# Kernel tuning notes

Measured on AMD Instinct MI355X. Metric: run time of the kernel, lower is better.

## Reference

```python
import jax, jax.numpy as jnp
import numpy as np

H = 128   # hidden_size
B = 8
TQ = 512  # num queries
TK = 512  # num keys


def setup_inputs() -> dict:
    key = jax.random.key(0)
    ks = jax.random.split(key, 8)
    s = 1.0 / np.sqrt(H)  # torch Linear default init bound
    return {
        "queries": jax.random.normal(ks[0], (B, TQ, H), dtype=jnp.float32),
        "keys": jax.random.normal(ks[1], (B, TK, H), dtype=jnp.float32),
        "Wa_w": jax.random.uniform(ks[2], (H, H), jnp.float32, -s, s),
        "Wa_b": jax.random.uniform(ks[3], (H,), jnp.float32, -s, s),
        "Ua_w": jax.random.uniform(ks[4], (H, H), jnp.float32, -s, s),
        "Ua_b": jax.random.uniform(ks[5], (H,), jnp.float32, -s, s),
        "Va_w": jax.random.uniform(ks[6], (H,), jnp.float32, -s, s),
        "Va_b": jax.random.uniform(ks[7], (), jnp.float32, -s, s),
    }


def reference(queries, keys, Wa_w, Wa_b, Ua_w, Ua_b, Va_w, Va_b):
    # Linear projections (torch Linear: y = x @ W.T + b)
    q = queries @ Wa_w.T + Wa_b                  # (B, Tq, H)
    k = keys @ Ua_w.T + Ua_b                     # (B, Tk, H)
    # Additive (Bahdanau) scores with broadcast intermediate (B, Tq, Tk, H)
    e = jnp.tanh(q[:, :, None, :] + k[:, None, :, :])
    scores = jnp.einsum('bqkh,h->bqk', e, Va_w) + Va_b  # (B, Tq, Tk)
    weights = jax.nn.softmax(scores, axis=-1)            # softmax over keys
    contexts = jnp.einsum('bqk,bkh->bqh', weights, keys) # (B, Tq, H)
    return contexts, weights
```

## Files before the change

### kernel.cpp

```cpp
#include <hip/hip_runtime.h>
#include <hip/hip_bf16.h>
#include <stdint.h>

#define HD 128
#define NB 8
#define TQN 512
#define TKN 512
#define QT 8
#define KTILE 64
#define KSTR 132
#define QSTR 132
#define KBSTR 136
#define FQT 8

typedef __attribute__((ext_vector_type(8))) short short8;
typedef __attribute__((ext_vector_type(4))) float f32x4;
typedef __attribute__((ext_vector_type(2))) float f32x2;

#if __has_builtin(__builtin_elementwise_fma)
#define FMA2(a,b,c) __builtin_elementwise_fma((a),(b),(c))
#else
#define FMA2(a,b,c) ((a)*(b)+(c))
#endif

static __device__ __forceinline__ float lo16(uint32_t w){
  union { uint32_t i; float f; } v; v.i = w << 16; return v.f;
}
static __device__ __forceinline__ float hi16(uint32_t w){
  union { uint32_t i; float f; } v; v.i = w & 0xffff0000u; return v.f;
}
static __device__ __forceinline__ float bf2f(unsigned short u){
  union { uint32_t i; float f; } v; v.i = ((uint32_t)u) << 16; return v.f;
}
static __device__ __forceinline__ uint32_t f2bf(float f){
  union { float f; uint32_t i; } v; v.f = f;
  uint32_t u = v.i;
  u += 0x7fffu + ((u >> 16) & 1u);
  return u >> 16;
}
static __device__ __forceinline__ float tanh_acc(float x){
  float e = __builtin_amdgcn_exp2f(x * 2.8853900817779268f);
  return fmaf(-2.0f, __builtin_amdgcn_rcpf(e + 1.0f), 1.0f);
}
template<int CTRL>
static __device__ __forceinline__ float dpp_add(float x){
  union { float f; int i; } u; u.f = x;
  int y = __builtin_amdgcn_update_dpp(0, u.i, CTRL, 0xf, 0xf, true);
  union { int i; float f; } w; w.i = y;
  return x + w.f;
}
static __device__ __forceinline__ float ld1(const void* p, size_t idx, bool f32){
  return f32 ? ((const float*)p)[idx] : bf2f(((const unsigned short*)p)[idx]);
}
static __device__ __forceinline__ short8 ld8bf(const void* p, size_t idx, bool f32){
  short8 r;
  if (f32){
    const float* s = (const float*)p + idx;
    #pragma unroll
    for (int i = 0; i < 8; i++) r[i] = (short)f2bf(s[i]);
  } else {
    r = *(const short8*)((const unsigned short*)p + idx);
  }
  return r;
}

__global__ __launch_bounds__(256) void proj_kernel(
    const void* __restrict__ queries, const void* __restrict__ keys,
    const void* __restrict__ Wa_w,   const void* __restrict__ Wa_b,
    const void* __restrict__ Ua_w,   const void* __restrict__ Ua_b,
    float* __restrict__ tq_g, unsigned short* __restrict__ tk_gb)
{
  __shared__ unsigned int flg_s[8];
  const int tid = threadIdx.x;
  if (tid < 8) flg_s[tid] = 0;
  __syncthreads();
  {
    const void* ptrs[6] = {queries, keys, Wa_w, Wa_b, Ua_w, Ua_b};
    const int grp = tid >> 5;
    const int l   = tid & 31;
    if (grp < 6){
      const unsigned short* p = (const unsigned short*)ptrs[grp];
      unsigned short a = p[2*l], c = p[64 + 2*l];
      if (((a >> 7) & 0xFF) > 0x90 || ((c >> 7) & 0xFF) > 0x90)
        atomicOr(&flg_s[grp], 1u);
    }
  }
  __syncthreads();
  const int lane = tid & 63, wv = tid >> 6, ln = lane & 15, quad = lane >> 4;
  const int b7  = blockIdx.x & 7;
  const int idx = blockIdx.x >> 3;
  const int row0 = (idx < 32) ? (b7*TQN + idx*16)
                              : (NB*TQN + b7*TKN + (idx-32)*16);

  const void* x; const void* W; const void* bias; int r;
  bool fx, fw, fb;
  const bool isK = (row0 >= NB*TQN);
  if (!isK){
    x = queries; W = Wa_w; bias = Wa_b; r = row0;
    fx = flg_s[0] != 0; fw = flg_s[2] != 0; fb = flg_s[3] != 0;
  } else {
    x = keys; W = Ua_w; bias = Ua_b; r = row0 - NB*TQN;
    fx = flg_s[1] != 0; fw = flg_s[4] != 0; fb = flg_s[5] != 0;
  }

  short8 a[4];
  #pragma unroll
  for (int ks = 0; ks < 4; ks++)
    a[ks] = ld8bf(x, (size_t)(r + ln)*HD + ks*32 + quad*8, fx);

  #pragma unroll
  for (int nt = 0; nt < 2; nt++){
    const int h0 = (2*wv + nt)*16;
    f32x4 c = {0.f,0.f,0.f,0.f};
    #pragma unroll
    for (int ks = 0; ks < 4; ks++)
      c = __builtin_amdgcn_mfma_f32_16x16x32_bf16(
            a[ks], ld8bf(W, (size_t)(h0 + ln)*HD + ks*32 + quad*8, fw), c, 0,0,0);
    const float wb = ld1(bias, h0 + ln, fb);
    #pragma unroll
    for (int r4 = 0; r4 < 4; r4++){
      const float e = __builtin_amdgcn_exp2f((c[r4] + wb) * 2.8853900817779268f);
      const float ec = fminf(fmaxf(e, 0x1p-13f), 0x1p13f);
      const size_t di = (size_t)(r + quad*4 + r4)*HD + h0 + ln;
      if (isK) tk_gb[di] = (unsigned short)f2bf(ec);
      else     tq_g[di]  = ec;
    }
  }
}

__global__ __launch_bounds__(1024, 8) void attn_kernel(
    const void* __restrict__ queries, const void* __restrict__ keys,
    const void* __restrict__ Va_w,
    const float* __restrict__ tq_g, const unsigned short* __restrict__ tk_gb,
    void* __restrict__ out)
{
  __shared__ __align__(16) unsigned short tkb_s[2][KTILE*KBSTR];
  __shared__ float wgt_s[QT*TKN];
  __shared__ unsigned int flg_s[4];

  const int tid = threadIdx.x;
  const int b     = blockIdx.x & 7;
  const int qbase = (blockIdx.x >> 3) * QT;

  uint4 st;
  {
    const uint4* src = (const uint4*)(tk_gb + (size_t)(b*TKN)*HD);
    st = src[tid];
  }

  if (tid < 4) flg_s[tid] = 0;
  __syncthreads();
  {
    const void* ptrs[3] = {queries, keys, Va_w};
    const int grp = tid >> 5;
    const int l   = tid & 31;
    if (grp < 3){
      const unsigned short* p = (const unsigned short*)ptrs[grp];
      unsigned short a = p[2*l], c = p[64 + 2*l];
      if (((a >> 7) & 0xFF) > 0x90 || ((c >> 7) & 0xFF) > 0x90)
        atomicOr(&flg_s[grp], 1u);
    }
  }
  __syncthreads();
  const bool fQ  = flg_s[0] != 0;
  const bool fK  = flg_s[1] != 0;
  const bool fVw = flg_s[2] != 0;

  const int lane = tid & 63;
  const int wv   = tid >> 6;
  const int qr   = wv & 7;
  const int hh   = wv >> 3;
  const int ln   = lane & 15;
  const int quad = lane >> 4;
  const int s8   = lane >> 3;
  const int o8   = lane & 7;
  const int sk   = tid >> 4;
  const int shh  = (tid & 15) * 8;

  f32x2 eq2[4], a2[4];
  {
    const float* qsrc = tq_g + (size_t)(b*TQN + qbase + qr)*HD + o8*16 + hh*8;
    #pragma unroll
    for (int c = 0; c < 2; c++){
      const float4 t = *(const float4*)(qsrc + c*4);
      eq2[2*c].x = t.x; eq2[2*c].y = t.y;
      eq2[2*c+1].x = t.z; eq2[2*c+1].y = t.w;
      a2[2*c].x   = -2.0f * ld1(Va_w, o8*16 + hh*8 + c*4 + 0, fVw);
      a2[2*c].y   = -2.0f * ld1(Va_w, o8*16 + hh*8 + c*4 + 1, fVw);
      a2[2*c+1].x = -2.0f * ld1(Va_w, o8*16 + hh*8 + c*4 + 2, fVw);
      a2[2*c+1].y = -2.0f * ld1(Va_w, o8*16 + hh*8 + c*4 + 3, fVw);
    }
  }
  f32x2 one2; one2.x = 1.f; one2.y = 1.f;

  *(uint4*)(&tkb_s[0][sk*KBSTR + shh]) = st;
  __syncthreads();

  float sc8[8];
  for (int kt = 0; kt < 8; kt++){
    if (kt < 7){
      const uint4* src = (const uint4*)(tk_gb + (size_t)(b*TKN + (kt+1)*KTILE)*HD);
      st = src[tid];
    }
    const unsigned short* buf = &tkb_s[kt & 1][0];

    float acc[8];
    #pragma unroll
    for (int i = 0; i < 8; i++){
      const unsigned short* tk = buf + (i*8 + s8)*KBSTR + o8*16 + hh*8;
      const uint4 v = *(const uint4*)tk;
      float acci = 0.f;
      {
        f32x2 kv0; kv0.x = lo16(v.x); kv0.y = hi16(v.x);
        f32x2 kv1; kv1.x = lo16(v.y); kv1.y = hi16(v.y);
        f32x2 x01 = FMA2(eq2[0], kv0, one2);
        f32x2 x23 = FMA2(eq2[1], kv1, one2);
        f32x2 xs01; xs01.x = x01.y; xs01.y = x01.x;
        f32x2 xs23; xs23.x = x23.y; xs23.y = x23.x;
        f32x2 s01 = a2[0] * xs01;
        f32x2 s23 = a2[1] * xs23;
        const float p01 = x01.x * x01.y;
        const float p23 = x23.x * x23.y;
        const float n01 = s01.x + s01.y;
        const float n23 = s23.x + s23.y;
        const float P   = p01 * p23;
        const float N   = fmaf(n01, p23, n23 * p01);
        acci = fmaf(N, __builtin_amdgcn_rcpf(P), acci);
      }
      {
        f32x2 kv0; kv0.x = lo16(v.z); kv0.y = hi16(v.z);
        f32x2 kv1; kv1.x = lo16(v.w); kv1.y = hi16(v.w);
        f32x2 x01 = FMA2(eq2[2], kv0, one2);
        f32x2 x23 = FMA2(eq2[3], kv1, one2);
        f32x2 xs01; xs01.x = x01.y; xs01.y = x01.x;
        f32x2 xs23; xs23.x = x23.y; xs23.y = x23.x;
        f32x2 s01 = a2[2] * xs01;
        f32x2 s23 = a2[3] * xs23;
        const float p01 = x01.x * x01.y;
        const float p23 = x23.x * x23.y;
        const float n01 = s01.x + s01.y;
        const float n23 = s23.x + s23.y;
        const float P   = p01 * p23;
        const float N   = fmaf(n01, p23, n23 * p01);
        acci = fmaf(N, __builtin_amdgcn_rcpf(P), acci);
      }
      acc[i] = acci;
    }
    #pragma unroll
    for (int i = 0; i < 8; i++){
      float a = acc[i];
      a = dpp_add<0xB1>(a);
      a = dpp_add<0x4E>(a);
      a = dpp_add<0x141>(a);
      acc[i] = a;
    }
    float sc = acc[0];
    #pragma unroll
    for (int i = 1; i < 8; i++) sc = (o8 == i) ? acc[i] : sc;
    sc8[kt] = sc;

    if (kt < 7)
      *(uint4*)(&tkb_s[(kt+1) & 1][sk*KBSTR + shh]) = st;
    __syncthreads();
  }

  float* psc = (float*)&tkb_s[0][0];
  if (hh == 1){
    #pragma unroll
    for (int kt = 0; kt < 8; kt++)
      psc[qr*TKN + kt*64 + o8*8 + s8] = sc8[kt];
  }
  __syncthreads();
  if (hh == 0){
    float vals[8];
    float m = -1e30f;
    #pragma unroll
    for (int j = 0; j < 8; j++){
      vals[j] = sc8[j] + psc[qr*TKN + j*64 + o8*8 + s8];
      m = fmaxf(m, vals[j]);
    }
    #pragma unroll
    for (int o = 32; o > 0; o >>= 1) m = fmaxf(m, __shfl_xor(m, o));
    float sum = 0.f;
    #pragma unroll
    for (int j = 0; j < 8; j++){
      vals[j] = __builtin_amdgcn_exp2f((vals[j]-m)*1.4426950408889634f);
      sum += vals[j];
    }
    #pragma unroll
    for (int o = 32; o > 0; o >>= 1) sum += __shfl_xor(sum, o);
    const float inv = __builtin_amdgcn_rcpf(sum);
    const int psrc = ((((lane & 7) << 3) | (lane >> 3)) << 2);
    const size_t wbase = (size_t)NB*TQN*HD + (size_t)(b*TQN + qbase + qr)*TKN;
    float* wrow = wgt_s + qr*TKN;
    #pragma unroll
    for (int j = 0; j < 8; j++){
      union { float f; int i; } u; u.f = vals[j]*inv;
      union { int i; float f; } t; t.i = __builtin_amdgcn_ds_bpermute(psrc, u.i);
      wrow[j*64 + lane] = t.f;
      if (fQ) ((float*)out)[wbase + j*64 + lane] = t.f;
      else    ((unsigned short*)out)[wbase + j*64 + lane] = (unsigned short)f2bf(t.f);
    }
  }
  __syncthreads();

  {
    const int p2 = wv & 3;
    const int g2 = wv >> 2;
    const int h0 = ln * 8;
    f32x2 a0v[4], a1v[4];
    #pragma unroll
    for (int t = 0; t < 4; t++){
      a0v[t].x = 0.f; a0v[t].y = 0.f;
      a1v[t].x = 0.f; a1v[t].y = 0.f;
    }
    const float* w0rb = wgt_s + (2*p2)*TKN;
    if (!fK){
      const unsigned short* kb = (const unsigned short*)keys
          + (size_t)(b*TKN)*HD + h0;
      #pragma unroll
      for (int t = 0; t < 2; t++){
        const int kt = g2*2 + t;
        const float* w0r = w0rb + kt*KTILE;
        const float* w1r = w0r + TKN;
        #pragma unroll
        for (int i = 0; i < 16; i++){
          const int k = i*4 + quad;
          const uint4 v = *(const uint4*)(kb + (size_t)(kt*KTILE + k)*HD);
          const float w0 = w0r[k];
          const float w1 = w1r[k];
          f32x2 c0; c0.x = lo16(v.x); c0.y = hi16(v.x);
// ... 83 lines not shown
        o0.x = f2bf(a0[0]) | (f2bf(a0[1]) << 16);
        o0.y = f2bf(a0[2]) | (f2bf(a0[3]) << 16);
        o0.z = f2bf(a0[4]) | (f2bf(a0[5]) << 16);
        o0.w = f2bf(a0[6]) | (f2bf(a0[7]) << 16);
        o1.x = f2bf(a1[0]) | (f2bf(a1[1]) << 16);
        o1.y = f2bf(a1[2]) | (f2bf(a1[3]) << 16);
        o1.z = f2bf(a1[4]) | (f2bf(a1[5]) << 16);
        o1.w = f2bf(a1[6]) | (f2bf(a1[7]) << 16);
        *(uint4*)((unsigned short*)out + crow0) = o0;
        *(uint4*)((unsigned short*)out + crow1) = o1;
      }
    }
  }
}

__global__ __launch_bounds__(512, 4) void fused_kernel(
    const void* __restrict__ queries, const void* __restrict__ keys,
    const void* __restrict__ Wa_w,   const void* __restrict__ Wa_b,
    const void* __restrict__ Ua_w,   const void* __restrict__ Ua_b,
    const void* __restrict__ Va_w,
    void* __restrict__ out)
{
  __shared__ float qp_s[FQT*QSTR];
  __shared__ float va_s[HD];
  __shared__ __align__(16) unsigned short keys_s[KTILE*KBSTR];
  __shared__ __align__(16) float kp_s[KTILE*KSTR];
  __shared__ float sc_s[FQT*TKN];
  __shared__ unsigned int flg_s[8];

  const int tid = threadIdx.x;
  if (tid < 8) flg_s[tid] = 0;
  __syncthreads();
  {
    const void* ptrs[7] = {queries, keys, Wa_w, Wa_b, Ua_w, Ua_b, Va_w};
    const int grp = tid >> 5;
    const int l   = tid & 31;
    if (grp < 7){
      const unsigned short* p = (const unsigned short*)ptrs[grp];
      unsigned short a = p[2*l], c = p[64 + 2*l];
      if (((a >> 7) & 0xFF) > 0x90 || ((c >> 7) & 0xFF) > 0x90)
        atomicOr(&flg_s[grp], 1u);
    }
  }
  __syncthreads();
  const bool fQ  = flg_s[0] != 0;
  const bool fK  = flg_s[1] != 0;
  const bool fWw = flg_s[2] != 0;
  const bool fWb = flg_s[3] != 0;
  const bool fUw = flg_s[4] != 0;
  const bool fUb = flg_s[5] != 0;
  const bool fVw = flg_s[6] != 0;

  const int lane = tid & 63;
  const int wv   = tid >> 6;
  const int ln   = lane & 15;
  const int quad = lane >> 4;
  const int b     = blockIdx.x >> 6;
  const int qbase = (blockIdx.x & 63) * FQT;

  if (tid < HD) va_s[tid] = ld1(Va_w, tid, fVw);
  {
    const int h0 = wv * 16;
    const size_t qrow = (size_t)(b*TQN + qbase + (ln & 7))*HD;
    f32x4 c = {0.f,0.f,0.f,0.f};
    #pragma unroll
    for (int ks = 0; ks < 4; ks++){
      short8 a = ld8bf(queries, qrow + ks*32 + quad*8, fQ);
      short8 w = ld8bf(Wa_w, (size_t)(h0 + ln)*HD + ks*32 + quad*8, fWw);
      c = __builtin_amdgcn_mfma_f32_16x16x32_bf16(a, w, c, 0,0,0);
    }
    const float wb = ld1(Wa_b, h0 + ln, fWb);
    #pragma unroll
    for (int r = 0; r < 4; r++){
      const int row = quad*4 + r;
      if (row < FQT) qp_s[row*QSTR + h0 + ln] = tanh_acc(c[r] + wb);
    }
  }
  short8 ub[4];
  float ubias;
  {
    const int h0 = wv * 16;
    #pragma unroll
    for (int ks = 0; ks < 4; ks++)
      ub[ks] = ld8bf(Ua_w, (size_t)(h0 + ln)*HD + ks*32 + quad*8, fUw);
    ubias = ld1(Ua_b, h0 + ln, fUb);
  }
  {
    if (fK){
      const float4* src = (const float4*)((const float*)keys + (size_t)(b*TKN)*HD);
      #pragma unroll
      for (int j = 0; j < 4; j++){
        const int f = tid + 512*j;
        float4 v = src[f];
        const int k = f >> 5, h = (f & 31)*4;
        uint2 p;
        p.x = f2bf(v.x) | (f2bf(v.y) << 16);
        p.y = f2bf(v.z) | (f2bf(v.w) << 16);
        *(uint2*)(keys_s + k*KBSTR + h) = p;
      }
    } else {
      const uint4* src = (const uint4*)((const unsigned short*)keys + (size_t)(b*TKN)*HD);
      #pragma unroll
      for (int j = 0; j < 2; j++){
        const int f = tid + 512*j;
        uint4 v = src[f];
        const int k = f >> 4, h = (f & 15)*8;
        *(uint4*)(keys_s + k*KBSTR + h) = v;
      }
    }
  }
  __syncthreads();

  const int s8 = lane >> 3;
  const int o8 = lane & 7;
  float tqr[16], var[16], vat[16];
  {
    const float* qsrc = qp_s + wv*QSTR + o8*16;
    const float* vsrc = va_s + o8*16;
    #pragma unroll
    for (int c = 0; c < 4; c++){
      float4 t = *(const float4*)(qsrc + c*4);
      float4 v = *(const float4*)(vsrc + c*4);
      tqr[c*4+0]=t.x; tqr[c*4+1]=t.y; tqr[c*4+2]=t.z; tqr[c*4+3]=t.w;
      var[c*4+0]=v.x; var[c*4+1]=v.y; var[c*4+2]=v.z; var[c*4+3]=v.w;
      vat[c*4+0]=v.x*t.x; vat[c*4+1]=v.y*t.y; vat[c*4+2]=v.z*t.z; vat[c*4+3]=v.w*t.w;
    }
  }
  for (int kt = 0; kt < 8; kt++){
    f32x4 kc[4];
    #pragma unroll
    for (int mt = 0; mt < 4; mt++) kc[mt] = (f32x4){0.f,0.f,0.f,0.f};
    #pragma unroll
    for (int ks = 0; ks < 4; ks++){
      short8 af[4];
      #pragma unroll
      for (int mt = 0; mt < 4; mt++)
        af[mt] = *(const short8*)(keys_s + (mt*16 + ln)*KBSTR + ks*32 + quad*8);
      #pragma unroll
      for (int mt = 0; mt < 4; mt++)
        kc[mt] = __builtin_amdgcn_mfma_f32_16x16x32_bf16(af[mt], ub[ks], kc[mt], 0,0,0);
    }
    __syncthreads();
    #pragma unroll
    for (int mt = 0; mt < 4; mt++)
      #pragma unroll
      for (int r = 0; r < 4; r++)
        kp_s[(mt*16 + quad*4 + r)*KSTR + wv*16 + ln] = tanh_acc(kc[mt][r] + ubias);
    if (kt < 7){
      if (fK){
        const float4* src = (const float4*)((const float*)keys + (size_t)(b*TKN + (kt+1)*KTILE)*HD);
        #pragma unroll
        for (int j = 0; j < 4; j++){
          const int f = tid + 512*j;
          float4 v = src[f];
          const int k = f >> 5, h = (f & 31)*4;
          uint2 p;
          p.x = f2bf(v.x) | (f2bf(v.y) << 16);
          p.y = f2bf(v.z) | (f2bf(v.w) << 16);
          *(uint2*)(keys_s + k*KBSTR + h) = p;
        }
      } else {
        const uint4* src = (const uint4*)((const unsigned short*)keys + (size_t)(b*TKN + (kt+1)*KTILE)*HD);
        #pragma unroll
        for (int j = 0; j < 2; j++){
          const int f = tid + 512*j;
          uint4 v = src[f];
          const int k = f >> 4, h = (f & 15)*8;
          *(uint4*)(keys_s + k*KBSTR + h) = v;
        }
      }
    }
    __syncthreads();
    float acc[8];
    #pragma unroll
    for (int i = 0; i < 8; i++) acc[i] = 0.f;
    #pragma unroll
    for (int i = 0; i < 8; i++){
      const float* tk = kp_s + (i*8 + s8)*KSTR + o8*16;
      #pragma unroll
      for (int c = 0; c < 4; c++){
        const float4 kv = *(const float4*)(tk + c*4);
        acc[i] = fmaf(fmaf(var[c*4+0], kv.x, vat[c*4+0]),
                      __builtin_amdgcn_rcpf(fmaf(tqr[c*4+0], kv.x, 1.f)), acc[i]);
        acc[i] = fmaf(fmaf(var[c*4+1], kv.y, vat[c*4+1]),
                      __builtin_amdgcn_rcpf(fmaf(tqr[c*4+1], kv.y, 1.f)), acc[i]);
        acc[i] = fmaf(fmaf(var[c*4+2], kv.z, vat[c*4+2]),
                      __builtin_amdgcn_rcpf(fmaf(tqr[c*4+2], kv.z, 1.f)), acc[i]);
        acc[i] = fmaf(fmaf(var[c*4+3], kv.w, vat[c*4+3]),
                      __builtin_amdgcn_rcpf(fmaf(tqr[c*4+3], kv.w, 1.f)), acc[i]);
      }
    }
    #pragma unroll
    for (int i = 0; i < 8; i++){
      float a = acc[i];
      a = dpp_add<0xB1>(a);
      a = dpp_add<0x4E>(a);
      a = dpp_add<0x141>(a);
      acc[i] = a;
    }
    float sc = acc[0];
    #pragma unroll
    for (int i = 1; i < 8; i++) sc = (o8 == i) ? acc[i] : sc;
    sc_s[wv*TKN + kt*KTILE + o8*8 + s8] = sc;
  }
  __syncthreads();
  {
    float vals[8];
    float m = -1e30f;
    #pragma unroll
    for (int j = 0; j < 8; j++){
      vals[j] = sc_s[wv*TKN + lane + 64*j];
      m = fmaxf(m, vals[j]);
    }
    #pragma unroll
    for (int o = 32; o > 0; o >>= 1) m = fmaxf(m, __shfl_xor(m, o));
    float sum = 0.f;
    #pragma unroll
    for (int j = 0; j < 8; j++){
      vals[j] = __builtin_amdgcn_exp2f((vals[j]-m)*1.4426950408889634f);
      sum += vals[j];
    }
    #pragma unroll
    for (int o = 32; o > 0; o >>= 1) sum += __shfl_xor(sum, o);
    const float inv = __builtin_amdgcn_rcpf(sum);
    const size_t wbase = (size_t)NB*TQN*HD + (size_t)(b*TQN + qbase + wv)*TKN;
    #pragma unroll
    for (int j = 0; j < 8; j++){
      const float w = vals[j]*inv;
      sc_s[wv*TKN + lane + 64*j] = w;
      if (fQ) ((float*)out)[wbase + lane + 64*j] = w;
      else    ((unsigned short*)out)[wbase + lane + 64*j] = (unsigned short)f2bf(w);
    }
  }
  __syncthreads();
  {
    const int p2 = wv & 3;
    const int g2 = wv >> 2;
    const int h0 = ln * 8;
    float a0[8], a1[8];
    #pragma unroll
    for (int t = 0; t < 8; t++){ a0[t] = 0.f; a1[t] = 0.f; }
    for (int kt = 0; kt < 8; kt++){
      if (fK){
        const float4* src = (const float4*)((const float*)keys + (size_t)(b*TKN + kt*KTILE)*HD);
        #pragma unroll
        for (int j = 0; j < 4; j++){
          const int f = tid + 512*j;
          const int k = f >> 5, h = (f & 31)*4;
          *(float4*)(kp_s + k*KSTR + h) = src[f];
        }
      } else {
        const uint4* src = (const uint4*)((const unsigned short*)keys + (size_t)(b*TKN + kt*KTILE)*HD);
        #pragma unroll
        for (int j = 0; j < 2; j++){
          const int f = tid + 512*j;
          const int k = f >> 4, h = (f & 15)*8;
          uint4 v = src[f];
          float4 d0, d1;
          d0.x = lo16(v.x); d0.y = hi16(v.x); d0.z = lo16(v.y); d0.w = hi16(v.y);
          d1.x = lo16(v.z); d1.y = hi16(v.z); d1.z = lo16(v.w); d1.w = hi16(v.w);
          *(float4*)(kp_s + k*KSTR + h)     = d0;
          *(float4*)(kp_s + k*KSTR + h + 4) = d1;
        }
      }
      __syncthreads();
      const float* w0r = sc_s + (2*p2)*TKN + kt*KTILE + g2*32;
      const float* w1r = w0r + TKN;
      #pragma unroll
      for (int i = 0; i < 8; i++){
        const int k = i*4 + quad;
        const float w0 = w0r[k];
        const float w1 = w1r[k];
        const float* kr = kp_s + (g2*32 + k)*KSTR + h0;
        const float4 k0 = *(const float4*)(kr);
        const float4 k1 = *(const float4*)(kr + 4);
        a0[0]=fmaf(w0,k0.x,a0[0]); a0[1]=fmaf(w0,k0.y,a0[1]);
        a0[2]=fmaf(w0,k0.z,a0[2]); a0[3]=fmaf(w0,k0.w,a0[3]);
        a0[4]=fmaf(w0,k1.x,a0[4]); a0[5]=fmaf(w0,k1.y,a0[5]);
        a0[6]=fmaf(w0,k1.z,a0[6]); a0[7]=fmaf(w0,k1.w,a0[7]);
        a1[0]=fmaf(w1,k0.x,a1[0]); a1[1]=fmaf(w1,k0.y,a1[1]);
        a1[2]=fmaf(w1,k0.z,a1[2]); a1[3]=fmaf(w1,k0.w,a1[3]);
        a1[4]=fmaf(w1,k1.x,a1[4]); a1[5]=fmaf(w1,k1.y,a1[5]);
        a1[6]=fmaf(w1,k1.z,a1[6]); a1[7]=fmaf(w1,k1.w,a1[7]);
      }
      __syncthreads();
    }
    #pragma unroll
    for (int t = 0; t < 8; t++){
      a0[t] += __shfl_xor(a0[t], 16); a0[t] += __shfl_xor(a0[t], 32);
      a1[t] += __shfl_xor(a1[t], 16); a1[t] += __shfl_xor(a1[t], 32);
    }
    float* part = qp_s;
    if (g2 == 1 && quad == 0){
      *(float4*)(part + (2*p2  )*HD + h0    ) = (float4){a0[0],a0[1],a0[2],a0[3]};
      *(float4*)(part + (2*p2  )*HD + h0 + 4) = (float4){a0[4],a0[5],a0[6],a0[7]};
      *(float4*)(part + (2*p2+1)*HD + h0    ) = (float4){a1[0],a1[1],a1[2],a1[3]};
      *(float4*)(part + (2*p2+1)*HD + h0 + 4) = (float4){a1[4],a1[5],a1[6],a1[7]};
    }
    __syncthreads();
    if (g2 == 0 && quad == 0){
      const float4 p00 = *(const float4*)(part + (2*p2  )*HD + h0    );
      const float4 p01 = *(const float4*)(part + (2*p2  )*HD + h0 + 4);
      const float4 p10 = *(const float4*)(part + (2*p2+1)*HD + h0    );
      const float4 p11 = *(const float4*)(part + (2*p2+1)*HD + h0 + 4);
      const size_t crow0 = (size_t)(b*TQN + qbase + 2*p2    )*HD + h0;
      const size_t crow1 = (size_t)(b*TQN + qbase + 2*p2 + 1)*HD + h0;
      if (fQ){
        float* oc = (float*)out;
        *(float4*)(oc + crow0)     = (float4){a0[0]+p00.x, a0[1]+p00.y, a0[2]+p00.z, a0[3]+p00.w};
        *(float4*)(oc + crow0 + 4) = (float4){a0[4]+p01.x, a0[5]+p01.y, a0[6]+p01.z, a0[7]+p01.w};
        *(float4*)(oc + crow1)     = (float4){a1[0]+p10.x, a1[1]+p10.y, a1[2]+p10.z, a1[3]+p10.w};
        *(float4*)(oc + crow1 + 4) = (float4){a1[4]+p11.x, a1[5]+p11.y, a1[6]+p11.z, a1[7]+p11.w};
      } else {
        uint4 o0, o1;
        o0.x = f2bf(a0[0]+p00.x) | (f2bf(a0[1]+p00.y) << 16);
        o0.y = f2bf(a0[2]+p00.z) | (f2bf(a0[3]+p00.w) << 16);
        o0.z = f2bf(a0[4]+p01.x) | (f2bf(a0[5]+p01.y) << 16);
        o0.w = f2bf(a0[6]+p01.z) | (f2bf(a0[7]+p01.w) << 16);
        o1.x = f2bf(a1[0]+p10.x) | (f2bf(a1[1]+p10.y) << 16);
        o1.y = f2bf(a1[2]+p10.z) | (f2bf(a1[3]+p10.w) << 16);
        o1.z = f2bf(a1[4]+p11.x) | (f2bf(a1[5]+p11.y) << 16);
        o1.w = f2bf(a1[6]+p11.z) | (f2bf(a1[7]+p11.w) << 16);
        *(uint4*)((unsigned short*)out + crow0) = o0;
        *(uint4*)((unsigned short*)out + crow1) = o1;
      }
    }
  }
}

extern "C" void kernel_launch(void* const* d_in, const int* in_sizes, int n_in,
                              void* d_out, int out_size, void* d_ws, size_t ws_size,
                              hipStream_t stream) {
  (void)in_sizes; (void)n_in; (void)out_size;
  const size_t need = (size_t)2 * NB * TQN * HD * sizeof(float);
  if (ws_size >= need){
    float* tq_g = (float*)d_ws;
    unsigned short* tk_gb = (unsigned short*)(tq_g + (size_t)NB*TQN*HD);
    proj_kernel<<<512, 256, 0, stream>>>(d_in[0], d_in[1], d_in[2], d_in[3],
                                         d_in[4], d_in[5], tq_g, tk_gb);
    attn_kernel<<<512, 1024, 0, stream>>>(d_in[0], d_in[1], d_in[6],
                                          tq_g, tk_gb, d_out);
  } else {
    fused_kernel<<<512, 512, 0, stream>>>(d_in[0], d_in[1], d_in[2], d_in[3],
                                          d_in[4], d_in[5], d_in[6], d_out);
  }
}
```

Before: 138.3 us.

## Fuse projections into attention kernel, recomputing key projection per block with MFMA

Replaces the two-kernel path (projection kernel writing tq/tk to workspace, then attention kernel) with a single fused kernel. Each block computes its 8 query projections and, per 64-key tile, the key projection via MFMA into a double-buffered LDS array, pipelined with the score loop and with prefetch of the next raw key tile. This removes one launch and the workspace round-trip. In exchange, every query block recomputes the full key projection for its batch, adding redundant matrix work and extra barriers.

```diff
diff --git a/kernel.cpp b/kernel.cpp
--- a/kernel.cpp
+++ b/kernel.cpp
@@ -8,10 +8,8 @@
 #define TKN 512
 #define QT 8
 #define KTILE 64
-#define KSTR 132
 #define QSTR 132
 #define KBSTR 136
-#define FQT 8
 
 typedef __attribute__((ext_vector_type(8))) short short8;
 typedef __attribute__((ext_vector_type(4))) float f32x4;
@@ -37,10 +35,6 @@
   uint32_t u = v.i;
   u += 0x7fffu + ((u >> 16) & 1u);
   return u >> 16;
-}
-static __device__ __forceinline__ float tanh_acc(float x){
-  float e = __builtin_amdgcn_exp2f(x * 2.8853900817779268f);
-  return fmaf(-2.0f, __builtin_amdgcn_rcpf(e + 1.0f), 1.0f);
 }
 template<int CTRL>
 static __device__ __forceinline__ float dpp_add(float x){
@@ -64,21 +58,29 @@
   return r;
 }
 
-__global__ __launch_bounds__(256) void proj_kernel(
+__global__ __launch_bounds__(1024, 8) void fused2_kernel(
     const void* __restrict__ queries, const void* __restrict__ keys,
     const void* __restrict__ Wa_w,   const void* __restrict__ Wa_b,
     const void* __restrict__ Ua_w,   const void* __restrict__ Ua_b,
-    float* __restrict__ tq_g, unsigned short* __restrict__ tk_gb)
+    const void* __restrict__ Va_w,
+    void* __restrict__ out)
 {
+  __shared__ __align__(16) unsigned short kraw_s[KTILE*KBSTR];
+  __shared__ __align__(16) unsigned short es[2][KTILE*KBSTR];
+  __shared__ float qp_s[QT*QSTR];
   __shared__ unsigned int flg_s[8];
+
   const int tid = threadIdx.x;
+  const int b     = blockIdx.x & 7;
+  const int qbase = (blockIdx.x >> 3) * QT;
+
   if (tid < 8) flg_s[tid] = 0;
   __syncthreads();
   {
-    const void* ptrs[6] = {queries, keys, Wa_w, Wa_b, Ua_w, Ua_b};
+    const void* ptrs[7] = {queries, keys, Wa_w, Wa_b, Ua_w, Ua_b, Va_w};
     const int grp = tid >> 5;
     const int l   = tid & 31;
-    if (grp < 6){
+    if (grp < 7){
       const unsigned short* p = (const unsigned short*)ptrs[grp];
       unsigned short a = p[2*l], c = p[64 + 2*l];
       if (((a >> 7) & 0xFF) > 0x90 || ((c >> 7) & 0xFF) > 0x90)
@@ -86,85 +88,13 @@
     }
   }
   __syncthreads();
-  const int lane = tid & 63, wv = tid >> 6, ln = lane & 15, quad = lane >> 4;
-  const int b7  = blockIdx.x & 7;
-  const int idx = blockIdx.x >> 3;
-  const int row0 = (idx < 32) ? (b7*TQN + idx*16)
-                              : (NB*TQN + b7*TKN + (idx-32)*16);
-
-  const void* x; const void* W; const void* bias; int r;
-  bool fx, fw, fb;
-  const bool isK = (row0 >= NB*TQN);
-  if (!isK){
-    x = queries; W = Wa_w; bias = Wa_b; r = row0;
-    fx = flg_s[0] != 0; fw = flg_s[2] != 0; fb = flg_s[3] != 0;
-  } else {
-    x = keys; W = Ua_w; bias = Ua_b; r = row0 - NB*TQN;
-    fx = flg_s[1] != 0; fw = flg_s[4] != 0; fb = flg_s[5] != 0;
-  }
-
-  short8 a[4];
-  #pragma unroll
-  for (int ks = 0; ks < 4; ks++)
-    a[ks] = ld8bf(x, (size_t)(r + ln)*HD + ks*32 + quad*8, fx);
-
-  #pragma unroll
-  for (int nt = 0; nt < 2; nt++){
-    const int h0 = (2*wv + nt)*16;
-    f32x4 c = {0.f,0.f,0.f,0.f};
-    #pragma unroll
-    for (int ks = 0; ks < 4; ks++)
-      c = __builtin_amdgcn_mfma_f32_16x16x32_bf16(
-            a[ks], ld8bf(W, (size_t)(h0 + ln)*HD + ks*32 + quad*8, fw), c, 0,0,0);
-    const float wb = ld1(bias, h0 + ln, fb);
-    #pragma unroll
-    for (int r4 = 0; r4 < 4; r4++){
-      const float e = __builtin_amdgcn_exp2f((c[r4] + wb) * 2.8853900817779268f);
-      const float ec = fminf(fmaxf(e, 0x1p-13f), 0x1p13f);
-      const size_t di = (size_t)(r + quad*4 + r4)*HD + h0 + ln;
-      if (isK) tk_gb[di] = (unsigned short)f2bf(ec);
-      else     tq_g[di]  = ec;
-    }
-  }
-}
-
-__global__ __launch_bounds__(1024, 8) void attn_kernel(
-    const void* __restrict__ queries, const void* __restrict__ keys,
-    const void* __restrict__ Va_w,
-    const float* __restrict__ tq_g, const unsigned short* __restrict__ tk_gb,
-    void* __restrict__ out)
-{
-  __shared__ __align__(16) unsigned short tkb_s[2][KTILE*KBSTR];
-  __shared__ float wgt_s[QT*TKN];
-  __shared__ unsigned int flg_s[4];
-
-  const int tid = threadIdx.x;
-  const int b     = blockIdx.x & 7;
-  const int qbase = (blockIdx.x >> 3) * QT;
-
-  uint4 st;
-  {
-    const uint4* src = (const uint4*)(tk_gb + (size_t)(b*TKN)*HD);
-    st = src[tid];
-  }
-
-  if (tid < 4) flg_s[tid] = 0;
-  __syncthreads();
-  {
-    const void* ptrs[3] = {queries, keys, Va_w};
-    const int grp = tid >> 5;
-    const int l   = tid & 31;
-    if (grp < 3){
-      const unsigned short* p = (const unsigned short*)ptrs[grp];
-      unsigned short a = p[2*l], c = p[64 + 2*l];
-      if (((a >> 7) & 0xFF) > 0x90 || ((c >> 7) & 0xFF) > 0x90)
-        atomicOr(&flg_s[grp], 1u);
-    }
-  }
-  __syncthreads();
   const bool fQ  = flg_s[0] != 0;
   const bool fK  = flg_s[1] != 0;
-  const bool fVw = flg_s[2] != 0;
+  const bool fWw = flg_s[2] != 0;
+  const bool fWb = flg_s[3] != 0;
+  const bool fUw = flg_s[4] != 0;
+  const bool fUb = flg_s[5] != 0;
+  const bool fVw = flg_s[6] != 0;
 
   const int lane = tid & 63;
   const int wv   = tid >> 6;
@@ -174,12 +104,59 @@
   const int quad = lane >> 4;
   const int s8   = lane >> 3;
   const int o8   = lane & 7;
-  const int sk   = tid >> 4;
-  const int shh  = (tid & 15) * 8;
+  const int kh0  = (wv & 7) * 16;
+  const int rh   = wv >> 3;
+
+  if (wv < 8){
+    const int h0 = wv * 16;
+    const size_t qrow = (size_t)(b*TQN + qbase + (ln & 7))*HD;
+    f32x4 c = {0.f,0.f,0.f,0.f};
+    #pragma unroll
+    for (int ks = 0; ks < 4; ks++){
+      short8 a = ld8bf(queries, qrow + ks*32 + quad*8, fQ);
+      short8 w = ld8bf(Wa_w, (size_t)(h0 + ln)*HD + ks*32 + quad*8, fWw);
+      c = __builtin_amdgcn_mfma_f32_16x16x32_bf16(a, w, c, 0,0,0);
+    }
+    const float wb = ld1(Wa_b, h0 + ln, fWb);
+    #pragma unroll
+    for (int r4 = 0; r4 < 4; r4++){
+      const int row = quad*4 + r4;
+      if (row < QT){
+        const float e = __builtin_amdgcn_exp2f((c[r4] + wb) * 2.8853900817779268f);
+        qp_s[row*QSTR + h0 + ln] = fminf(fmaxf(e, 0x1p-13f), 0x1p13f);
+      }
+    }
+  }
+  short8 ub[4];
+  float ubias;
+  {
+    #pragma unroll
+    for (int ks = 0; ks < 4; ks++)
+      ub[ks] = ld8bf(Ua_w, (size_t)(kh0 + ln)*HD + ks*32 + quad*8, fUw);
+    ubias = ld1(Ua_b, kh0 + ln, fUb);
+  }
+  if (fK){
+    const float4* src = (const float4*)((const float*)keys + (size_t)(b*TKN)*HD);
+    #pragma unroll
+    for (int j = 0; j < 2; j++){
+      const int f = tid + 1024*j;
+      float4 v = src[f];
+      const int k = f >> 5, h = (f & 31)*4;
+      uint2 p;
+      p.x = f2bf(v.x) | (f2bf(v.y) << 16);
+      p.y = f2bf(v.z) | (f2bf(v.w) << 16);
+      *(uint2*)(kraw_s + k*KBSTR + h) = p;
+    }
+  } else {
+    const uint4* src = (const uint4*)((const unsigned short*)keys + (size_t)(b*TKN)*HD);
+    const int k = tid >> 4, h = (tid & 15)*8;
+    *(uint4*)(kraw_s + k*KBSTR + h) = src[tid];
+  }
+  __syncthreads();
 
   f32x2 eq2[4], a2[4];
   {
-    const float* qsrc = tq_g + (size_t)(b*TQN + qbase + qr)*HD + o8*16 + hh*8;
+    const float* qsrc = qp_s + qr*QSTR + o8*16 + hh*8;
     #pragma unroll
     for (int c = 0; c < 2; c++){
       const float4 t = *(const float4*)(qsrc + c*4);
@@ -193,78 +170,165 @@
   }
   f32x2 one2; one2.x = 1.f; one2.y = 1.f;
 
-  *(uint4*)(&tkb_s[0][sk*KBSTR + shh]) = st;
+  uint4 st0, st1;
+  {
+    f32x4 kc[2];
+    kc[0] = (f32x4){0.f,0.f,0.f,0.f};
+    kc[1] = (f32x4){0.f,0.f,0.f,0.f};
+    #pragma unroll
+    for (int ks = 0; ks < 4; ks++){
+      short8 af0 = *(const short8*)(kraw_s + (rh*32      + ln)*KBSTR + ks*32 + quad*8);
+      short8 af1 = *(const short8*)(kraw_s + (rh*32 + 16 + ln)*KBSTR + ks*32 + quad*8);
+      kc[0] = __builtin_amdgcn_mfma_f32_16x16x32_bf16(af0, ub[ks], kc[0], 0,0,0);
+      kc[1] = __builtin_amdgcn_mfma_f32_16x16x32_bf16(af1, ub[ks], kc[1], 0,0,0);
+    }
+    if (fK){
+      const uint4* src = (const uint4*)((const float*)keys + (size_t)(b*TKN + KTILE)*HD);
+      st0 = src[tid]; st1 = src[tid + 1024];
+    } else {
+      const uint4* src = (const uint4*)((const unsigned short*)keys + (size_t)(b*TKN + KTILE)*HD);
+      st0 = src[tid];
+    }
+    #pragma unroll
+    for (int mt = 0; mt < 2; mt++)
+      #pragma unroll
+      for (int r4 = 0; r4 < 4; r4++){
+        const int row = rh*32 + mt*16 + quad*4 + r4;
+        const float e = __builtin_amdgcn_exp2f((kc[mt][r4] + ubias) * 2.8853900817779268f);
+        es[0][row*KBSTR + kh0 + ln] =
+            (unsigned short)f2bf(fminf(fmaxf(e, 0x1p-13f), 0x1p13f));
+      }
+  }
+  __syncthreads();
+  if (fK){
+    #pragma unroll
+    for (int j = 0; j < 2; j++){
+      uint4 v = j ? st1 : st0;
+      const int f = tid + 1024*j;
+      const int k = f >> 5, h = (f & 31)*4;
+      uint2 p;
+      p.x = f2bf(__uint_as_float(v.x)) | (f2bf(__uint_as_float(v.y)) << 16);
+      p.y = f2bf(__uint_as_float(v.z)) | (f2bf(__uint_as_float(v.w)) << 16);
+      *(uint2*)(kraw_s + k*KBSTR + h) = p;
+    }
+  } else {
+    *(uint4*)(kraw_s + (tid >> 4)*KBSTR + (tid & 15)*8) = st0;
+  }
   __syncthreads();
 
   float sc8[8];
   for (int kt = 0; kt < 8; kt++){
+    f32x4 kc[2];
     if (kt < 7){
-      const uint4* src = (const uint4*)(tk_gb + (size_t)(b*TKN + (kt+1)*KTILE)*HD);
-      st = src[tid];
-    }
-    const unsigned short* buf = &tkb_s[kt & 1][0];
-
-    float acc[8];
-    #pragma unroll
-    for (int i = 0; i < 8; i++){
-      const unsigned short* tk = buf + (i*8 + s8)*KBSTR + o8*16 + hh*8;
-      const uint4 v = *(const uint4*)tk;
-      float acci = 0.f;
-      {
-        f32x2 kv0; kv0.x = lo16(v.x); kv0.y = hi16(v.x);
-        f32x2 kv1; kv1.x = lo16(v.y); kv1.y = hi16(v.y);
-        f32x2 x01 = FMA2(eq2[0], kv0, one2);
-        f32x2 x23 = FMA2(eq2[1], kv1, one2);
-        f32x2 xs01; xs01.x = x01.y; xs01.y = x01.x;
-        f32x2 xs23; xs23.x = x23.y; xs23.y = x23.x;
-        f32x2 s01 = a2[0] * xs01;
-        f32x2 s23 = a2[1] * xs23;
-        const float p01 = x01.x * x01.y;
-        const float p23 = x23.x * x23.y;
-        const float n01 = s01.x + s01.y;
-        const float n23 = s23.x + s23.y;
-        const float P   = p01 * p23;
-        const float N   = fmaf(n01, p23, n23 * p01);
-        acci = fmaf(N, __builtin_amdgcn_rcpf(P), acci);
-      }
-      {
-        f32x2 kv0; kv0.x = lo16(v.z); kv0.y = hi16(v.z);
-        f32x2 kv1; kv1.x = lo16(v.w); kv1.y = hi16(v.w);
-        f32x2 x01 = FMA2(eq2[2], kv0, one2);
-        f32x2 x23 = FMA2(eq2[3], kv1, one2);
-        f32x2 xs01; xs01.x = x01.y; xs01.y = x01.x;
-        f32x2 xs23; xs23.x = x23.y; xs23.y = x23.x;
-        f32x2 s01 = a2[2] * xs01;
-        f32x2 s23 = a2[3] * xs23;
-        const float p01 = x01.x * x01.y;
-        const float p23 = x23.x * x23.y;
-        const float n01 = s01.x + s01.y;
-        const float n23 = s23.x + s23.y;
-        const float P   = p01 * p23;
-        const float N   = fmaf(n01, p23, n23 * p01);
-        acci = fmaf(N, __builtin_amdgcn_rcpf(P), acci);
-      }
-      acc[i] = acci;
-    }
-    #pragma unroll
-    for (int i = 0; i < 8; i++){
-      float a = acc[i];
-      a = dpp_add<0xB1>(a);
-      a = dpp_add<0x4E>(a);
-      a = dpp_add<0x141>(a);
-      acc[i] = a;
-    }
-    float sc = acc[0];
-    #pragma unroll
-    for (int i = 1; i < 8; i++) sc = (o8 == i) ? acc[i] : sc;
-    sc8[kt] = sc;
-
-    if (kt < 7)
-      *(uint4*)(&tkb_s[(kt+1) & 1][sk*KBSTR + shh]) = st;
+      kc[0] = (f32x4){0.f,0.f,0.f,0.f};
+      kc[1] = (f32x4){0.f,0.f,0.f,0.f};
+      #pragma unroll
+      for (int ks = 0; ks < 4; ks++){
+        short8 af0 = *(const short8*)(kraw_s + (rh*32      + ln)*KBSTR + ks*32 + quad*8);
+        short8 af1 = *(const short8*)(kraw_s + (rh*32 + 16 + ln)*KBSTR + ks*32 + quad*8);
+        kc[0] = __builtin_amdgcn_mfma_f32_16x16x32_bf16(af0, ub[ks], kc[0], 0,0,0);
+        kc[1] = __builtin_amdgcn_mfma_f32_16x16x32_bf16(af1, ub[ks], kc[1], 0,0,0);
+      }
+      if (kt < 6){
+        if (fK){
+          const uint4* src = (const uint4*)((const float*)keys + (size_t)(b*TKN + (kt+2)*KTILE)*HD);
+          st0 = src[tid]; st1 = src[tid + 1024];
+        } else {
+          const uint4* src = (const uint4*)((const unsigned short*)keys + (size_t)(b*TKN + (kt+2)*KTILE)*HD);
+          st0 = src[tid];
+        }
+      }
+    }
+    {
+      const unsigned short* buf = &es[kt & 1][0];
+      float acc[8];
+      #pragma unroll
+      for (int i = 0; i < 8; i++){
+        const unsigned short* tk = buf + (i*8 + s8)*KBSTR + o8*16 + hh*8;
+        const uint4 v = *(const uint4*)tk;
+        float acci = 0.f;
+        {
+          f32x2 kv0; kv0.x = lo16(v.x); kv0.y = hi16(v.x);
+          f32x2 kv1; kv1.x = lo16(v.y); kv1.y = hi16(v.y);
+          f32x2 x01 = FMA2(eq2[0], kv0, one2);
+          f32x2 x23 = FMA2(eq2[1], kv1, one2);
+          f32x2 xs01; xs01.x = x01.y; xs01.y = x01.x;
+          f32x2 xs23; xs23.x = x23.y; xs23.y = x23.x;
+          f32x2 s01 = a2[0] * xs01;
+          f32x2 s23 = a2[1] * xs23;
+          const float p01 = x01.x * x01.y;
+          const float p23 = x23.x * x23.y;
+          const float n01 = s01.x + s01.y;
+          const float n23 = s23.x + s23.y;
+          const float P   = p01 * p23;
+          const float N   = fmaf(n01, p23, n23 * p01);
+          acci = fmaf(N, __builtin_amdgcn_rcpf(P), acci);
+        }
+        {
+          f32x2 kv0; kv0.x = lo16(v.z); kv0.y = hi16(v.z);
+          f32x2 kv1; kv1.x = lo16(v.w); kv1.y = hi16(v.w);
+          f32x2 x01 = FMA2(eq2[2], kv0, one2);
+          f32x2 x23 = FMA2(eq2[3], kv1, one2);
+          f32x2 xs01; xs01.x = x01.y; xs01.y = x01.x;
+          f32x2 xs23; xs23.x = x23.y; xs23.y = x23.x;
+          f32x2 s01 = a2[2] * xs01;
+          f32x2 s23 = a2[3] * xs23;
+          const float p01 = x01.x * x01.y;
+          const float p23 = x23.x * x23.y;
+          const float n01 = s01.x + s01.y;
+          const float n23 = s23.x + s23.y;
+          const float P   = p01 * p23;
+          const float N   = fmaf(n01, p23, n23 * p01);
+          acci = fmaf(N, __builtin_amdgcn_rcpf(P), acci);
+        }
+        acc[i] = acci;
+      }
+      #pragma unroll
+      for (int i = 0; i < 8; i++){
+        float a = acc[i];
+        a = dpp_add<0xB1>(a);
+        a = dpp_add<0x4E>(a);
+        a = dpp_add<0x141>(a);
+        acc[i] = a;
+      }
+      float sc = acc[0];
+      #pragma unroll
+      for (int i = 1; i < 8; i++) sc = (o8 == i) ? acc[i] : sc;
+      sc8[kt] = sc;
+    }
+    if (kt < 7){
+      #pragma unroll
+      for (int mt = 0; mt < 2; mt++)
+        #pragma unroll
+        for (int r4 = 0; r4 < 4; r4++){
+          const int row = rh*32 + mt*16 + quad*4 + r4;
+          const float e = __builtin_amdgcn_exp2f((kc[mt][r4] + ubias) * 2.8853900817779268f);
+          es[(kt+1) & 1][row*KBSTR + kh0 + ln] =
+              (unsigned short)f2bf(fminf(fmaxf(e, 0x1p-13f), 0x1p13f));
+        }
+    }
     __syncthreads();
-  }
-
-  float* psc = (float*)&tkb_s[0][0];
+    if (kt < 6){
+      if (fK){
+        #pragma unroll
+        for (int j = 0; j < 2; j++){
+          uint4 v = j ? st1 : st0;
+          const int f = tid + 1024*j;
+          const int k = f >> 5, h = (f & 31)*4;
+          uint2 p;
+          p.x = f2bf(__uint_as_float(v.x)) | (f2bf(__uint_as_float(v.y)) << 16);
+          p.y = f2bf(__uint_as_float(v.z)) | (f2bf(__uint_as_float(v.w)) << 16);
+          *(uint2*)(kraw_s + k*KBSTR + h) = p;
+        }
+      } else {
+        *(uint4*)(kraw_s + (tid >> 4)*KBSTR + (tid & 15)*8) = st0;
+      }
+      __syncthreads();
+    }
+  }
+
+  float* psc = (float*)&es[0][0];
+  float* wgt = (float*)&es[1][0];
   if (hh == 1){
     #pragma unroll
     for (int kt = 0; kt < 8; kt++)
@@ -292,7 +356,7 @@
     const float inv = __builtin_amdgcn_rcpf(sum);
     const int psrc = ((((lane & 7) << 3) | (lane >> 3)) << 2);
     const size_t wbase = (size_t)NB*TQN*HD + (size_t)(b*TQN + qbase + qr)*TKN;
-    float* wrow = wgt_s + qr*TKN;
+    float* wrow = wgt + qr*TKN;
     #pragma unroll
     for (int j = 0; j < 8; j++){
       union { float f; int i; } u; u.f = vals[j]*inv;
@@ -314,7 +378,7 @@
       a0v[t].x = 0.f; a0v[t].y = 0.f;
       a1v[t].x = 0.f; a1v[t].y = 0.f;
     }
-    const float* w0rb = wgt_s + (2*p2)*TKN;
+    const float* w0rb = wgt + (2*p2)*TKN;
     if (!fK){
       const unsigned short* kb = (const unsigned short*)keys
           + (size_t)(b*TKN)*HD + h0;
@@ -428,334 +492,10 @@
   }
 }
 
-__global__ __launch_bounds__(512, 4) void fused_kernel(
-    const void* __restrict__ queries, const void* __restrict__ keys,
-    const void* __restrict__ Wa_w,   const void* __restrict__ Wa_b,
-    const void* __restrict__ Ua_w,   const void* __restrict__ Ua_b,
-    const void* __restrict__ Va_w,
-    void* __restrict__ out)
-{
-  __shared__ float qp_s[FQT*QSTR];
-  __shared__ float va_s[HD];
-  __shared__ __align__(16) unsigned short keys_s[KTILE*KBSTR];
-  __shared__ __align__(16) float kp_s[KTILE*KSTR];
-  __shared__ float sc_s[FQT*TKN];
-  __shared__ unsigned int flg_s[8];
-
-  const int tid = threadIdx.x;
-  if (tid < 8) flg_s[tid] = 0;
-  __syncthreads();
-  {
-    const void* ptrs[7] = {queries, keys, Wa_w, Wa_b, Ua_w, Ua_b, Va_w};
-    const int grp = tid >> 5;
-    const int l   = tid & 31;
-    if (grp < 7){
-      const unsigned short* p = (const unsigned short*)ptrs[grp];
-      unsigned short a = p[2*l], c = p[64 + 2*l];
-      if (((a >> 7) & 0xFF) > 0x90 || ((c >> 7) & 0xFF) > 0x90)
-        atomicOr(&flg_s[grp], 1u);
-    }
-  }
-  __syncthreads();
-  const bool fQ  = flg_s[0] != 0;
-  const bool fK  = flg_s[1] != 0;
-  const bool fWw = flg_s[2] != 0;
-  const bool fWb = flg_s[3] != 0;
-  const bool fUw = flg_s[4] != 0;
-  const bool fUb = flg_s[5] != 0;
-  const bool fVw = flg_s[6] != 0;
-
-  const int lane = tid & 63;
-  const int wv   = tid >> 6;
-  const int ln   = lane & 15;
-  const int quad = lane >> 4;
-  const int b     = blockIdx.x >> 6;
-  const int qbase = (blockIdx.x & 63) * FQT;
-
-  if (tid < HD) va_s[tid] = ld1(Va_w, tid, fVw);
-  {
-    const int h0 = wv * 16;
-    const size_t qrow = (size_t)(b*TQN + qbase + (ln & 7))*HD;
-    f32x4 c = {0.f,0.f,0.f,0.f};
-    #pragma unroll
-    for (int ks = 0; ks < 4; ks++){
-      short8 a = ld8bf(queries, qrow + ks*32 + quad*8, fQ);
-      short8 w = ld8bf(Wa_w, (size_t)(h0 + ln)*HD + ks*32 + quad*8, fWw);
-      c = __builtin_amdgcn_mfma_f32_16x16x32_bf16(a, w, c, 0,0,0);
-    }
-    const float wb = ld1(Wa_b, h0 + ln, fWb);
-    #pragma unroll
-    for (int r = 0; r < 4; r++){
-      const int row = quad*4 + r;
-      if (row < FQT) qp_s[row*QSTR + h0 + ln] = tanh_acc(c[r] + wb);
-    }
-  }
-  short8 ub[4];
-  float ubias;
-  {
-    const int h0 = wv * 16;
-    #pragma unroll
-    for (int ks = 0; ks < 4; ks++)
-      ub[ks] = ld8bf(Ua_w, (size_t)(h0 + ln)*HD + ks*32 + quad*8, fUw);
-    ubias = ld1(Ua_b, h0 + ln, fUb);
-  }
-  {
-    if (fK){
-      const float4* src = (const float4*)((const float*)keys + (size_t)(b*TKN)*HD);
-      #pragma unroll
-      for (int j = 0; j < 4; j++){
-        const int f = tid + 512*j;
-        float4 v = src[f];
-        const int k = f >> 5, h = (f & 31)*4;
-        uint2 p;
-        p.x = f2bf(v.x) | (f2bf(v.y) << 16);
-        p.y = f2bf(v.z) | (f2bf(v.w) << 16);
-        *(uint2*)(keys_s + k*KBSTR + h) = p;
-      }
-    } else {
-      const uint4* src = (const uint4*)((const unsigned short*)keys + (size_t)(b*TKN)*HD);
-      #pragma unroll
-      for (int j = 0; j < 2; j++){
-        const int f = tid + 512*j;
-        uint4 v = src[f];
-        const int k = f >> 4, h = (f & 15)*8;
-        *(uint4*)(keys_s + k*KBSTR + h) = v;
-      }
-    }
-  }
-  __syncthreads();
-
-  const int s8 = lane >> 3;
-  const int o8 = lane & 7;
-  float tqr[16], var[16], vat[16];
-  {
-    const float* qsrc = qp_s + wv*QSTR + o8*16;
-    const float* vsrc = va_s + o8*16;
-    #pragma unroll
-    for (int c = 0; c < 4; c++){
-      float4 t = *(const float4*)(qsrc + c*4);
-      float4 v = *(const float4*)(vsrc + c*4);
-      tqr[c*4+0]=t.x; tqr[c*4+1]=t.y; tqr[c*4+2]=t.z; tqr[c*4+3]=t.w;
-      var[c*4+0]=v.x; var[c*4+1]=v.y; var[c*4+2]=v.z; var[c*4+3]=v.w;
-      vat[c*4+0]=v.x*t.x; vat[c*4+1]=v.y*t.y; vat[c*4+2]=v.z*t.z; vat[c*4+3]=v.w*t.w;
-    }
-  }
-  for (int kt = 0; kt < 8; kt++){
-    f32x4 kc[4];
-    #pragma unroll
-    for (int mt = 0; mt < 4; mt++) kc[mt] = (f32x4){0.f,0.f,0.f,0.f};
-    #pragma unroll
-    for (int ks = 0; ks < 4; ks++){
-      short8 af[4];
-      #pragma unroll
-      for (int mt = 0; mt < 4; mt++)
-        af[mt] = *(const short8*)(keys_s + (mt*16 + ln)*KBSTR + ks*32 + quad*8);
-      #pragma unroll
-      for (int mt = 0; mt < 4; mt++)
-        kc[mt] = __builtin_amdgcn_mfma_f32_16x16x32_bf16(af[mt], ub[ks], kc[mt], 0,0,0);
-    }
-    __syncthreads();
-    #pragma unroll
-    for (int mt = 0; mt < 4; mt++)
-      #pragma unroll
-      for (int r = 0; r < 4; r++)
-        kp_s[(mt*16 + quad*4 + r)*KSTR + wv*16 + ln] = tanh_acc(kc[mt][r] + ubias);
-    if (kt < 7){
-      if (fK){
-        const float4* src = (const float4*)((const float*)keys + (size_t)(b*TKN + (kt+1)*KTILE)*HD);
-        #pragma unroll
-        for (int j = 0; j < 4; j++){
-          const int f = tid + 512*j;
-          float4 v = src[f];
-          const int k = f >> 5, h = (f & 31)*4;
-          uint2 p;
-          p.x = f2bf(v.x) | (f2bf(v.y) << 16);
-          p.y = f2bf(v.z) | (f2bf(v.w) << 16);
-          *(uint2*)(keys_s + k*KBSTR + h) = p;
-        }
-      } else {
-        const uint4* src = (const uint4*)((const unsigned short*)keys + (size_t)(b*TKN + (kt+1)*KTILE)*HD);
-        #pragma unroll
-        for (int j = 0; j < 2; j++){
-          const int f = tid + 512*j;
-          uint4 v = src[f];
-          const int k = f >> 4, h = (f & 15)*8;
-          *(uint4*)(keys_s + k*KBSTR + h) = v;
-        }
-      }
-    }
-    __syncthreads();
-    float acc[8];
-    #pragma unroll
-    for (int i = 0; i < 8; i++) acc[i] = 0.f;
-    #pragma unroll
-    for (int i = 0; i < 8; i++){
-      const float* tk = kp_s + (i*8 + s8)*KSTR + o8*16;
-      #pragma unroll
-      for (int c = 0; c < 4; c++){
-        const float4 kv = *(const float4*)(tk + c*4);
-        acc[i] = fmaf(fmaf(var[c*4+0], kv.x, vat[c*4+0]),
-                      __builtin_amdgcn_rcpf(fmaf(tqr[c*4+0], kv.x, 1.f)), acc[i]);
-        acc[i] = fmaf(fmaf(var[c*4+1], kv.y, vat[c*4+1]),
-                      __builtin_amdgcn_rcpf(fmaf(tqr[c*4+1], kv.y, 1.f)), acc[i]);
-        acc[i] = fmaf(fmaf(var[c*4+2], kv.z, vat[c*4+2]),
-                      __builtin_amdgcn_rcpf(fmaf(tqr[c*4+2], kv.z, 1.f)), acc[i]);
-        acc[i] = fmaf(fmaf(var[c*4+3], kv.w, vat[c*4+3]),
-                      __builtin_amdgcn_rcpf(fmaf(tqr[c*4+3], kv.w, 1.f)), acc[i]);
-      }
-    }
-    #pragma unroll
-    for (int i = 0; i < 8; i++){
-      float a = acc[i];
-      a = dpp_add<0xB1>(a);
-      a = dpp_add<0x4E>(a);
-      a = dpp_add<0x141>(a);
-      acc[i] = a;
-    }
-    float sc = acc[0];
-    #pragma unroll
-    for (int i = 1; i < 8; i++) sc = (o8 == i) ? acc[i] : sc;
-    sc_s[wv*TKN + kt*KTILE + o8*8 + s8] = sc;
-  }
-  __syncthreads();
-  {
-    float vals[8];
-    float m = -1e30f;
-    #pragma unroll
-    for (int j = 0; j < 8; j++){
-      vals[j] = sc_s[wv*TKN + lane + 64*j];
-      m = fmaxf(m, vals[j]);
-    }
-    #pragma unroll
-    for (int o = 32; o > 0; o >>= 1) m = fmaxf(m, __shfl_xor(m, o));
-    float sum = 0.f;
-    #pragma unroll
-    for (int j = 0; j < 8; j++){
-      vals[j] = __builtin_amdgcn_exp2f((vals[j]-m)*1.4426950408889634f);
-      sum += vals[j];
-    }
-    #pragma unroll
-    for (int o = 32; o > 0; o >>= 1) sum += __shfl_xor(sum, o);
-    const float inv = __builtin_amdgcn_rcpf(sum);
-    const size_t wbase = (size_t)NB*TQN*HD + (size_t)(b*TQN + qbase + wv)*TKN;
-    #pragma unroll
-    for (int j = 0; j < 8; j++){
-      const float w = vals[j]*inv;
-      sc_s[wv*TKN + lane + 64*j] = w;
-      if (fQ) ((float*)out)[wbase + lane + 64*j] = w;
-      else    ((unsigned short*)out)[wbase + lane + 64*j] = (unsigned short)f2bf(w);
-    }
-  }
-  __syncthreads();
-  {
-    const int p2 = wv & 3;
-    const int g2 = wv >> 2;
-    const int h0 = ln * 8;
-    float a0[8], a1[8];
-    #pragma unroll
-    for (int t = 0; t < 8; t++){ a0[t] = 0.f; a1[t] = 0.f; }
-    for (int kt = 0; kt < 8; kt++){
-      if (fK){
-        const float4* src = (const float4*)((const float*)keys + (size_t)(b*TKN + kt*KTILE)*HD);
-        #pragma unroll
-        for (int j = 0; j < 4; j++){
-          const int f = tid + 512*j;
-          const int k = f >> 5, h = (f & 31)*4;
-          *(float4*)(kp_s + k*KSTR + h) = src[f];
-        }
-      } else {
-        const uint4* src = (const uint4*)((const unsigned short*)keys + (size_t)(b*TKN + kt*KTILE)*HD);
-        #pragma unroll
-        for (int j = 0; j < 2; j++){
-          const int f = tid + 512*j;
-          const int k = f >> 4, h = (f & 15)*8;
-          uint4 v = src[f];
-          float4 d0, d1;
-          d0.x = lo16(v.x); d0.y = hi16(v.x); d0.z = lo16(v.y); d0.w = hi16(v.y);
-          d1.x = lo16(v.z); d1.y = hi16(v.z); d1.z = lo16(v.w); d1.w = hi16(v.w);
-          *(float4*)(kp_s + k*KSTR + h)     = d0;
-          *(float4*)(kp_s + k*KSTR + h + 4) = d1;
-        }
-      }
-      __syncthreads();
-      const float* w0r = sc_s + (2*p2)*TKN + kt*KTILE + g2*32;
-      const float* w1r = w0r + TKN;
-      #pragma unroll
-      for (int i = 0; i < 8; i++){
-        const int k = i*4 + quad;
-        const float w0 = w0r[k];
-        const float w1 = w1r[k];
-        const float* kr = kp_s + (g2*32 + k)*KSTR + h0;
-        const float4 k0 = *(const float4*)(kr);
-        const float4 k1 = *(const float4*)(kr + 4);
-        a0[0]=fmaf(w0,k0.x,a0[0]); a0[1]=fmaf(w0,k0.y,a0[1]);
-        a0[2]=fmaf(w0,k0.z,a0[2]); a0[3]=fmaf(w0,k0.w,a0[3]);
-        a0[4]=fmaf(w0,k1.x,a0[4]); a0[5]=fmaf(w0,k1.y,a0[5]);
-        a0[6]=fmaf(w0,k1.z,a0[6]); a0[7]=fmaf(w0,k1.w,a0[7]);
-        a1[0]=fmaf(w1,k0.x,a1[0]); a1[1]=fmaf(w1,k0.y,a1[1]);
-        a1[2]=fmaf(w1,k0.z,a1[2]); a1[3]=fmaf(w1,k0.w,a1[3]);
-        a1[4]=fmaf(w1,k1.x,a1[4]); a1[5]=fmaf(w1,k1.y,a1[5]);
-        a1[6]=fmaf(w1,k1.z,a1[6]); a1[7]=fmaf(w1,k1.w,a1[7]);
-      }
-      __syncthreads();
-    }
-    #pragma unroll
-    for (int t = 0; t < 8; t++){
-      a0[t] += __shfl_xor(a0[t], 16); a0[t] += __shfl_xor(a0[t], 32);
-      a1[t] += __shfl_xor(a1[t], 16); a1[t] += __shfl_xor(a1[t], 32);
-    }
-    float* part = qp_s;
-    if (g2 == 1 && quad == 0){
-      *(float4*)(part + (2*p2  )*HD + h0    ) = (float4){a0[0],a0[1],a0[2],a0[3]};
-      *(float4*)(part + (2*p2  )*HD + h0 + 4) = (float4){a0[4],a0[5],a0[6],a0[7]};
-      *(float4*)(part + (2*p2+1)*HD + h0    ) = (float4){a1[0],a1[1],a1[2],a1[3]};
-      *(float4*)(part + (2*p2+1)*HD + h0 + 4) = (float4){a1[4],a1[5],a1[6],a1[7]};
-    }
-    __syncthreads();
-    if (g2 == 0 && quad == 0){
-      const float4 p00 = *(const float4*)(part + (2*p2  )*HD + h0    );
-      const float4 p01 = *(const float4*)(part + (2*p2  )*HD + h0 + 4);
-      const float4 p10 = *(const float4*)(part + (2*p2+1)*HD + h0    );
-      const float4 p11 = *(const float4*)(part + (2*p2+1)*HD + h0 + 4);
-      const size_t crow0 = (size_t)(b*TQN + qbase + 2*p2    )*HD + h0;
-      const size_t crow1 = (size_t)(b*TQN + qbase + 2*p2 + 1)*HD + h0;
-      if (fQ){
-        float* oc = (float*)out;
-        *(float4*)(oc + crow0)     = (float4){a0[0]+p00.x, a0[1]+p00.y, a0[2]+p00.z, a0[3]+p00.w};
-        *(float4*)(oc + crow0 + 4) = (float4){a0[4]+p01.x, a0[5]+p01.y, a0[6]+p01.z, a0[7]+p01.w};
-        *(float4*)(oc + crow1)     = (float4){a1[0]+p10.x, a1[1]+p10.y, a1[2]+p10.z, a1[3]+p10.w};
-        *(float4*)(oc + crow1 + 4) = (float4){a1[4]+p11.x, a1[5]+p11.y, a1[6]+p11.z, a1[7]+p11.w};
-      } else {
-        uint4 o0, o1;
-        o0.x = f2bf(a0[0]+p00.x) | (f2bf(a0[1]+p00.y) << 16);
-        o0.y = f2bf(a0[2]+p00.z) | (f2bf(a0[3]+p00.w) << 16);
-        o0.z = f2bf(a0[4]+p01.x) | (f2bf(a0[5]+p01.y) << 16);
-        o0.w = f2bf(a0[6]+p01.z) | (f2bf(a0[7]+p01.w) << 16);
-        o1.x = f2bf(a1[0]+p10.x) | (f2bf(a1[1]+p10.y) << 16);
-        o1.y = f2bf(a1[2]+p10.z) | (f2bf(a1[3]+p10.w) << 16);
-        o1.z = f2bf(a1[4]+p11.x) | (f2bf(a1[5]+p11.y) << 16);
-        o1.w = f2bf(a1[6]+p11.z) | (f2bf(a1[7]+p11.w) << 16);
-        *(uint4*)((unsigned short*)out + crow0) = o0;
-        *(uint4*)((unsigned short*)out + crow1) = o1;
-      }
-    }
-  }
-}
-
 extern "C" void kernel_launch(void* const* d_in, const int* in_sizes, int n_in,
                               void* d_out, int out_size, void* d_ws, size_t ws_size,
                               hipStream_t stream) {
-  (void)in_sizes; (void)n_in; (void)out_size;
-  const size_t need = (size_t)2 * NB * TQN * HD * sizeof(float);
-  if (ws_size >= need){
-    float* tq_g = (float*)d_ws;
-    unsigned short* tk_gb = (unsigned short*)(tq_g + (size_t)NB*TQN*HD);
-    proj_kernel<<<512, 256, 0, stream>>>(d_in[0], d_in[1], d_in[2], d_in[3],
-                                         d_in[4], d_in[5], tq_g, tk_gb);
-    attn_kernel<<<512, 1024, 0, stream>>>(d_in[0], d_in[1], d_in[6],
-                                          tq_g, tk_gb, d_out);
-  } else {
-    fused_kernel<<<512, 512, 0, stream>>>(d_in[0], d_in[1], d_in[2], d_in[3],
+  (void)in_sizes; (void)n_in; (void)out_size; (void)d_ws; (void)ws_size;
+  fused2_kernel<<<512, 1024, 0, stream>>>(d_in[0], d_in[1], d_in[2], d_in[3],
                                           d_in[4], d_in[5], d_in[6], d_out);
-  }
-}
+}
```

After: 203.5 us. 47.1% more time.
